# Performance work log

Measured on AMD Instinct MI355X. Metric: run time of the kernel, lower is better.

The kernel has to match this reference:

```python
import jax, jax.numpy as jnp
import numpy as np

B, C, H, W = 2, 256, 64, 64
NUM_HEADS = 8


def setup_inputs() -> dict:
    key = jax.random.key(0)
    k1, k2, k3 = jax.random.split(key, 3)
    x = jax.random.normal(k1, (B, C, H, W), dtype=jnp.float32)
    # 1x1 convs, bias=False -> plain [out_ch, in_ch] matrices
    w_qkv = jax.random.normal(k2, (3 * C, C), dtype=jnp.float32) * (1.0 / np.sqrt(C))
    w_proj = jax.random.normal(k3, (C, C), dtype=jnp.float32) * (1.0 / np.sqrt(C))
    return {"x": x, "w_qkv": w_qkv, "w_proj": w_proj}


def reference(x, w_qkv, w_proj):
    b, c, h, w = x.shape
    hd = NUM_HEADS
    d = c // hd  # head dim
    n = h * w    # number of tokens

    # 1x1 conv == channel matmul: [3C, C] x [B, C, H, W] -> [B, 3C, H, W]
    qkv = jnp.einsum('oc,bchw->bohw', w_qkv, x)
    q, k, v = jnp.split(qkv, 3, axis=1)

    def reshape(t):
        return t.reshape(b, hd, d, n)  # [B, h, d, N]

    q, k, v = map(reshape, (q, k, v))

    # scores[b,h,i,j] = sum_d q[b,h,d,i] * k[b,h,d,j] / sqrt(d)
    scores = jnp.einsum('bhdi,bhdj->bhij', q, k) / jnp.sqrt(jnp.asarray(d, x.dtype))
    attn = jax.nn.softmax(scores, axis=-1)

    # out[b,h,d,i] = sum_j attn[b,h,i,j] * v[b,h,d,j]
    out = jnp.einsum('bhij,bhdj->bhdi', attn, v)
    out = out.reshape(b, c, h, w)

    return jnp.einsum('oc,bchw->bohw', w_proj, out) + x
```

## Files before the change

kernel.cpp:

```cpp
#include <hip/hip_runtime.h>
#include <hip/hip_bf16.h>

#define NB  2
#define CC  256
#define NHD 8
#define HD  32
#define NT  4096

typedef __bf16 bf16x8 __attribute__((ext_vector_type(8)));
typedef bf16x8 bf16x8_ma __attribute__((may_alias));
typedef __bf16 bf16x4 __attribute__((ext_vector_type(4)));
typedef bf16x4 bf16x4_ma __attribute__((may_alias));
typedef float  f32x4  __attribute__((ext_vector_type(4)));
typedef f32x4  f32x4_ma __attribute__((may_alias));
typedef float  f32x16 __attribute__((ext_vector_type(16)));
typedef unsigned int u32x4 __attribute__((ext_vector_type(4)));
typedef unsigned short u16x8 __attribute__((ext_vector_type(8)));

static __device__ __forceinline__ f32x4 zero4() {
    f32x4 z = {0.f, 0.f, 0.f, 0.f}; return z;
}
static __device__ __forceinline__ f32x16 zero16() {
    f32x16 z = {0.f,0.f,0.f,0.f,0.f,0.f,0.f,0.f,
                0.f,0.f,0.f,0.f,0.f,0.f,0.f,0.f};
    return z;
}

#define QSCALE 0.25505392421795654f

#define CVT_PK(dst, lo, hi_) \
    asm("v_cvt_pk_bf16_f32 %0, %1, %2" : "=v"(dst) : "v"(lo), "v"(hi_))
#define PLSWAP(x, y) \
    asm("v_permlane32_swap_b32 %0, %1" : "+v"(x), "+v"(y))


__global__ __launch_bounds__(256) void convw_k(const float* __restrict__ s1,
                                               __bf16* __restrict__ d1, int n1,
                                               const float* __restrict__ s2,
                                               __bf16* __restrict__ d2, int n2) {
    const int i = blockIdx.x * 256 + threadIdx.x;
    if (i < n1) d1[i] = (__bf16)s1[i];
    else if (i - n1 < n2) d2[i - n1] = (__bf16)s2[i - n1];
}

__global__ __launch_bounds__(256) void qkv_k(const __bf16* __restrict__ wqkv,
                                             const float* __restrict__ x,
                                             __bf16* __restrict__ qt,
                                             __bf16* __restrict__ kt,
                                             __bf16* __restrict__ vv) {
    __shared__ __align__(16) __bf16 T[64][264];

    const int tid  = threadIdx.x;
    const int lane = tid & 63, wv = tid >> 6;
    const int g = lane >> 4, c16 = lane & 15;
    const int b    = blockIdx.z;
    const int o0   = blockIdx.y * 64 + wv * 16;
    const int tok0 = blockIdx.x * 64;

    const int tok4 = (tid & 15) * 4;
    const int crow = tid >> 4;

    {
#pragma unroll
        for (int i = 0; i < 8; ++i) {
            const int c = i * 16 + crow;
            f32x4 v = *(const f32x4_ma*)&x[((size_t)(b * CC + c)) * NT + tok0 + tok4];
#pragma unroll
            for (int j = 0; j < 4; ++j) T[tok4 + j][c] = (__bf16)v[j];
        }
    }

    f32x4 v1[8];
#pragma unroll
    for (int i = 0; i < 8; ++i) {
        const int c = 128 + i * 16 + crow;
        v1[i] = *(const f32x4_ma*)&x[((size_t)(b * CC + c)) * NT + tok0 + tok4];
    }

    const __bf16* arow = wqkv + (size_t)(o0 + c16) * CC + g * 8;
    bf16x8 a[8];
#pragma unroll
    for (int kc = 0; kc < 8; ++kc) a[kc] = *(const bf16x8_ma*)(arow + kc * 32);

    __syncthreads();

    f32x4 acc[4];
#pragma unroll
    for (int i = 0; i < 4; ++i) acc[i] = zero4();

#pragma unroll
    for (int kc = 0; kc < 4; ++kc) {
#pragma unroll
        for (int js = 0; js < 4; ++js) {
            bf16x8 bb = *(const bf16x8_ma*)&T[js * 16 + c16][kc * 32 + g * 8];
            acc[js] = __builtin_amdgcn_mfma_f32_16x16x32_bf16(a[kc], bb, acc[js], 0, 0, 0);
        }
    }

#pragma unroll
    for (int i = 0; i < 8; ++i) {
        const int c = 128 + i * 16 + crow;
#pragma unroll
        for (int j = 0; j < 4; ++j) T[tok4 + j][c] = (__bf16)v1[i][j];
    }
    __syncthreads();

#pragma unroll
    for (int kc = 4; kc < 8; ++kc) {
#pragma unroll
        for (int js = 0; js < 4; ++js) {
            bf16x8 bb = *(const bf16x8_ma*)&T[js * 16 + c16][kc * 32 + g * 8];
            acc[js] = __builtin_amdgcn_mfma_f32_16x16x32_bf16(a[kc], bb, acc[js], 0, 0, 0);
        }
    }

    const int reg = o0 >> 8;
    const int oo0 = (o0 & 255) + g * 4;
    const int h   = oo0 >> 5;
    const int dd0 = oo0 & 31;
    const size_t bh = (size_t)(b * NHD + h);

#pragma unroll
    for (int js = 0; js < 4; ++js) {
        const int tok = tok0 + js * 16 + c16;
        if (reg == 0) {
            bf16x4 pk;
#pragma unroll
            for (int r = 0; r < 4; ++r) pk[r] = (__bf16)(acc[js][r] * QSCALE);
            *(bf16x4_ma*)(qt + (bh * NT + tok) * HD + dd0) = pk;
        } else if (reg == 1) {
            bf16x4 pk;
#pragma unroll
            for (int r = 0; r < 4; ++r) pk[r] = (__bf16)acc[js][r];
            *(bf16x4_ma*)(kt + (bh * NT + tok) * HD + dd0) = pk;
        } else {
#pragma unroll
            for (int r = 0; r < 4; ++r)
                vv[(bh * HD + dd0 + r) * NT + tok] = (__bf16)acc[js][r];
        }
    }
}

__global__ __launch_bounds__(256, 4) void attn_k(const __bf16* __restrict__ qt,
                                                 const __bf16* __restrict__ kt,
                                                 const __bf16* __restrict__ vv,
                                                 __bf16* __restrict__ ao,
                                                 float* __restrict__ PO,
                                                 float* __restrict__ PL) {
    __shared__ __align__(16) __bf16 KF[2][4][2][512];
    __shared__ __align__(16) __bf16 VF[2][4][2][512];

    const int tid  = threadIdx.x;
    const int lane = tid & 63, wv = tid >> 6;
    const int c32 = lane & 31, hi = lane >> 5;
    const int bh = blockIdx.y;
    const int b = bh >> 3, h = bh & 7;
    const int seg = blockIdx.z, nseg = gridDim.z;
    const int i0q = blockIdx.x * 128 + wv * 32;

    const __bf16* qbase = qt + ((size_t)bh * NT + i0q) * HD;
    const __bf16* kbase = kt + (size_t)bh * NT * HD;
    const __bf16* vbase = vv + (size_t)bh * HD * NT;

    bf16x8 aq0 = *(const bf16x8_ma*)(qbase + (size_t)c32 * HD + hi * 8);
    bf16x8 aq1 = *(const bf16x8_ma*)(qbase + (size_t)c32 * HD + 16 + hi * 8);

    u16x8 ones_u = {0x3F80,0x3F80,0x3F80,0x3F80,0x3F80,0x3F80,0x3F80,0x3F80};
    const bf16x8 ones = __builtin_bit_cast(bf16x8, ones_u);

    f32x16 oacc = zero16();
    f32x16 lacc = zero16();

#define STAGE(bf, jb) do {                                                              \
    const __bf16* gk = kbase + (size_t)((jb) + wv * 32 + c32) * HD + hi * 8;            \
    __builtin_amdgcn_global_load_lds(                                                   \
        (const __attribute__((address_space(1))) void*)gk,                              \
        (__attribute__((address_space(3))) void*)&KF[bf][wv][0][0],                     \
        16, 0, 0);                                                                      \
    __builtin_amdgcn_global_load_lds(                                                   \
        (const __attribute__((address_space(1))) void*)(gk + 16),                       \
        (__attribute__((address_space(3))) void*)&KF[bf][wv][1][0],                     \
        16, 0, 0);                                                                      \
    const __bf16* gv = vbase + (size_t)c32 * NT + (jb) + wv * 32 + hi * 8;              \
    __builtin_amdgcn_global_load_lds(                                                   \
        (const __attribute__((address_space(1))) void*)gv,                              \
        (__attribute__((address_space(3))) void*)&VF[bf][wv][0][0],                     \
        16, 0, 0);                                                                      \
    __builtin_amdgcn_global_load_lds(                                                   \
        (const __attribute__((address_space(1))) void*)(gv + 16),                       \
        (__attribute__((address_space(3))) void*)&VF[bf][wv][1][0],                     \
        16, 0, 0);                                                                      \
} while (0)

#define SUBTILE(bf, js) do {                                                            \
    bf16x8 fk0 = *(const bf16x8_ma*)&KF[bf][js][0][lane * 8];                           \
    bf16x8 fk1 = *(const bf16x8_ma*)&KF[bf][js][1][lane * 8];                           \
    bf16x8 fv0 = *(const bf16x8_ma*)&VF[bf][js][0][lane * 8];                           \
    bf16x8 fv1 = *(const bf16x8_ma*)&VF[bf][js][1][lane * 8];                           \
    f32x16 s = __builtin_amdgcn_mfma_f32_32x32x16_bf16(fk0, aq0, zero16(), 0, 0, 0);    \
    s = __builtin_amdgcn_mfma_f32_32x32x16_bf16(fk1, aq1, s, 0, 0, 0);                  \
    float p[16];                                                                        \
    _Pragma("unroll")                                                                   \
    for (int r = 0; r < 16; ++r) p[r] = __builtin_amdgcn_exp2f(s[r]);                   \
    unsigned pk[8];                                                                     \
    _Pragma("unroll")                                                                   \
    for (int i = 0; i < 8; ++i) CVT_PK(pk[i], p[2 * i], p[2 * i + 1]);                  \
    PLSWAP(pk[0], pk[2]);                                                               \
    PLSWAP(pk[1], pk[3]);                                                               \
    PLSWAP(pk[4], pk[6]);                                                               \
    PLSWAP(pk[5], pk[7]);                                                               \
    u32x4 a0 = {pk[0], pk[1], pk[2], pk[3]};                                            \
    u32x4 a1 = {pk[4], pk[5], pk[6], pk[7]};                                            \
    const bf16x8 ap0 = __builtin_bit_cast(bf16x8, a0);                                  \
    const bf16x8 ap1 = __builtin_bit_cast(bf16x8, a1);                                  \
    oacc = __builtin_amdgcn_mfma_f32_32x32x16_bf16(ap0, fv0, oacc, 0, 0, 0);            \
    oacc = __builtin_amdgcn_mfma_f32_32x32x16_bf16(ap1, fv1, oacc, 0, 0, 0);            \
    lacc = __builtin_amdgcn_mfma_f32_32x32x16_bf16(ap0, ones, lacc, 0, 0, 0);           \
    lacc = __builtin_amdgcn_mfma_f32_32x32x16_bf16(ap1, ones, lacc, 0, 0, 0);           \
} while (0)

    const int ntiles  = (NT / 128) / nseg;
    const int j_begin = seg * ntiles * 128;

    STAGE(0, j_begin);
    asm volatile("s_waitcnt vmcnt(0)" ::: "memory");
    __syncthreads();

    int buf = 0;
#pragma unroll 1
    for (int t = 0; t < ntiles; ++t) {
        if (t + 1 < ntiles) STAGE(buf ^ 1, j_begin + (t + 1) * 128);
        SUBTILE(buf, 0);
        SUBTILE(buf, 1);
        SUBTILE(buf, 2);
        SUBTILE(buf, 3);
        asm volatile("s_waitcnt vmcnt(0)" ::: "memory");
        __syncthreads();
        buf ^= 1;
    }

#undef STAGE
#undef SUBTILE

    if (nseg == 1) {
#pragma unroll
        for (int g4 = 0; g4 < 4; ++g4) {
#pragma unroll
            for (int r = 0; r < 4; ++r) {
                const int q = 8 * g4 + 4 * hi + r;
                ao[((size_t)(b * NT) + i0q + q) * CC + h * HD + c32] =
                    (__bf16)(oacc[4 * g4 + r] / lacc[4 * g4 + r]);
            }
        }
    } else {
        float* po = PO + (((size_t)seg * NB * NHD + bh) * NT + i0q) * HD;
#pragma unroll
        for (int g4 = 0; g4 < 4; ++g4) {
#pragma unroll
            for (int r = 0; r < 4; ++r) {
                const int q = 8 * g4 + 4 * hi + r;
                po[(size_t)q * HD + c32] = oacc[4 * g4 + r];
            }
        }
        if (c32 == 0) {
            float* pl = PL + ((size_t)seg * NB * NHD + bh) * NT + i0q;
#pragma unroll
            for (int g4 = 0; g4 < 4; ++g4)
#pragma unroll
                for (int r = 0; r < 4; ++r)
                    pl[8 * g4 + 4 * hi + r] = lacc[4 * g4 + r];
        }
    }
}

__global__ __launch_bounds__(256) void comb_k(const float* __restrict__ PO,
                                              const float* __restrict__ PL,
                                              __bf16* __restrict__ ao,
                                              int nseg) {
    const int i = blockIdx.x * 256 + threadIdx.x;
    const int bh = i >> 15;
    const int rem = i & 32767;
    const int n = rem >> 3, g = rem & 7;
    const int b = bh >> 3, h = bh & 7;

    const size_t SEGO = (size_t)(NB * NHD) * NT * HD;
    const size_t SEGL = (size_t)(NB * NHD) * NT;
    const size_t o0i = (((size_t)bh) * NT + n) * HD + g * 4;
    const size_t li  = (size_t)bh * NT + n;

    f32x4 o = *(const f32x4_ma*)&PO[o0i];
    float l = PL[li];
#pragma unroll 3
    for (int s = 1; s < nseg; ++s) {
        o += *(const f32x4_ma*)&PO[(size_t)s * SEGO + o0i];
        l += PL[(size_t)s * SEGL + li];
    }

    bf16x4 pk;
#pragma unroll
    for (int r = 0; r < 4; ++r) pk[r] = (__bf16)(o[r] / l);
    *(bf16x4_ma*)&ao[((size_t)(b * NT) + n) * CC + h * HD + g * 4] = pk;
}

__global__ __launch_bounds__(256) void proj_k(const __bf16* __restrict__ wp,
                                              const __bf16* __restrict__ ao,
                                              const float* __restrict__ x,
                                              float* __restrict__ out) {
    __shared__ __align__(16) __bf16 BF[4][8][512];

    const int lane = threadIdx.x & 63, wv = threadIdx.x >> 6;
    const int g = lane >> 4, c16 = lane & 15;
    const int b    = blockIdx.z;
    const int o0   = blockIdx.y * 64 + wv * 16;
    const int tok0 = blockIdx.x * 64;

    const __bf16* bsrc = ao + ((size_t)(b * NT + tok0 + wv * 16 + c16)) * CC + g * 8;
#pragma unroll
    for (int kc = 0; kc < 4; ++kc) {
        __builtin_amdgcn_global_load_lds(
            (const __attribute__((address_space(1))) void*)(bsrc + kc * 32),
            (__attribute__((address_space(3))) void*)&BF[wv][kc][0],
            16, 0, 0);
    }

    const __bf16* arow = wp + (size_t)(o0 + c16) * CC + g * 8;
    bf16x8 a[8];
#pragma unroll
    for (int kc = 0; kc < 8; ++kc) a[kc] = *(const bf16x8_ma*)(arow + kc * 32);

    __syncthreads();

#pragma unroll
    for (int kc = 4; kc < 8; ++kc) {
        __builtin_amdgcn_global_load_lds(
            (const __attribute__((address_space(1))) void*)(bsrc + kc * 32),
            (__attribute__((address_space(3))) void*)&BF[wv][kc][0],
            16, 0, 0);
    }

    f32x4 acc[4];
#pragma unroll
    for (int i = 0; i < 4; ++i) acc[i] = zero4();

#pragma unroll
    for (int kc = 0; kc < 4; ++kc) {
#pragma unroll
        for (int js = 0; js < 4; ++js) {
            bf16x8 bb = *(const bf16x8_ma*)&BF[js][kc][lane * 8];
            acc[js] = __builtin_amdgcn_mfma_f32_16x16x32_bf16(a[kc], bb, acc[js], 0, 0, 0);
        }
    }

    asm volatile("s_waitcnt vmcnt(0)" ::: "memory");
    __syncthreads();

#pragma unroll
    for (int kc = 4; kc < 8; ++kc) {
#pragma unroll
        for (int js = 0; js < 4; ++js) {
            bf16x8 bb = *(const bf16x8_ma*)&BF[js][kc][lane * 8];
            acc[js] = __builtin_amdgcn_mfma_f32_16x16x32_bf16(a[kc], bb, acc[js], 0, 0, 0);
        }
    }

#pragma unroll
    for (int js = 0; js < 4; ++js) {
        const int tok = tok0 + js * 16 + c16;
#pragma unroll
        for (int r = 0; r < 4; ++r) {
            const int o = o0 + g * 4 + r;
            const size_t idx = ((size_t)(b * CC + o)) * NT + tok;
            out[idx] = acc[js][r] + x[idx];
        }
    }
}

extern "C" void kernel_launch(void* const* d_in, const int* in_sizes, int n_in,
                              void* d_out, int out_size, void* d_ws, size_t ws_size,
                              hipStream_t stream) {
    const int SX  = NB * CC * NT;
    const int SW3 = 3 * CC * CC;
    const int SW1 = CC * CC;
    const size_t E = (size_t)SX;

    const float* x  = nullptr;
    const float* wq = nullptr;
    const float* wp = nullptr;
    for (int i = 0; i < n_in; ++i) {
        const int sz = in_sizes[i];
        if (sz == SX || sz == 2 * SX || sz == 4 * SX)           x  = (const float*)d_in[i];
        else if (sz == SW3 || sz == 2 * SW3 || sz == 4 * SW3)   wq = (const float*)d_in[i];
        else if (sz == SW1 || sz == 2 * SW1 || sz == 4 * SW1)   wp = (const float*)d_in[i];
    }
    if (!x || !wq || !wp) {
        x  = (const float*)d_in[0];
        wq = (const float*)d_in[1];
        wp = (const float*)d_in[2];
    }

    __bf16* ws  = (__bf16*)d_ws;
    __bf16* wqb = ws;
    __bf16* wpb = wqb + SW3;
    __bf16* ao  = wpb + SW1;
    __bf16* qt  = ao + E;
    __bf16* kt  = qt + E;
    __bf16* vv  = kt + E;

    const size_t baseB = (size_t)(SW3 + SW1) * 2 + 4 * E * 2;
    const size_t segoB = (size_t)NB * NHD * NT * HD * 4;
    const size_t seglB = (size_t)NB * NHD * NT * 4;
    const int jseg = (ws_size >= baseB + 2 * (segoB + seglB)) ? 2 : 1;
    float* PO = (float*)((char*)d_ws + baseB);
    float* PL = (float*)((char*)d_ws + baseB + (size_t)jseg * segoB);

    float* out = (float*)d_out;

    convw_k<<<dim3((SW3 + SW1 + 255) / 256), 256, 0, stream>>>(wq, wqb, SW3, wp, wpb, SW1);
    qkv_k<<<dim3(NT / 64, (3 * CC) / 64, NB), 256, 0, stream>>>(wqb, x, qt, kt, vv);
    attn_k<<<dim3(NT / 128, NB * NHD, jseg), 256, 0, stream>>>(qt, kt, vv, ao, PO, PL);
    if (jseg > 1)
        comb_k<<<dim3((NB * NHD * NT * (HD / 4)) / 256), 256, 0, stream>>>(PO, PL, ao, jseg);
    proj_k<<<dim3(NT / 64, CC / 64, NB), 256, 0, stream>>>(wpb, ao, x, out);
}
```

Before: 141.6 us.

## Process two query tiles per wave and replace ones-MFMA row sums with VALU sums

Each wave now handles 64 queries (two 32-row Q tiles) instead of 32, so each K/V fragment read from LDS is reused twice, and blocks shrink to 128 threads with each wave staging two subtiles. The softmax denominator, previously computed with two extra MFMAs against a ones matrix, is now accumulated with VALU adds on the exp values and reduced by cross-lane shuffles at the end. This removes a third of the MFMA work and halves LDS reads per unit of compute, in exchange for more registers per wave, fewer waves per block, and extra VALU adds alongside the exp work.

```diff
diff --git a/kernel.cpp b/kernel.cpp
--- a/kernel.cpp
+++ b/kernel.cpp
@@ -15,7 +15,6 @@
 typedef f32x4  f32x4_ma __attribute__((may_alias));
 typedef float  f32x16 __attribute__((ext_vector_type(16)));
 typedef unsigned int u32x4 __attribute__((ext_vector_type(4)));
-typedef unsigned short u16x8 __attribute__((ext_vector_type(8)));
 
 static __device__ __forceinline__ f32x4 zero4() {
     f32x4 z = {0.f, 0.f, 0.f, 0.f}; return z;
@@ -141,12 +140,12 @@
     }
 }
 
-__global__ __launch_bounds__(256, 4) void attn_k(const __bf16* __restrict__ qt,
-                                                 const __bf16* __restrict__ kt,
-                                                 const __bf16* __restrict__ vv,
-                                                 __bf16* __restrict__ ao,
-                                                 float* __restrict__ PO,
-                                                 float* __restrict__ PL) {
+__global__ __launch_bounds__(128) void attn_k(const __bf16* __restrict__ qt,
+                                              const __bf16* __restrict__ kt,
+                                              const __bf16* __restrict__ vv,
+                                              __bf16* __restrict__ ao,
+                                              float* __restrict__ PO,
+                                              float* __restrict__ PL) {
     __shared__ __align__(16) __bf16 KF[2][4][2][512];
     __shared__ __align__(16) __bf16 VF[2][4][2][512];
 
@@ -156,52 +155,56 @@
     const int bh = blockIdx.y;
     const int b = bh >> 3, h = bh & 7;
     const int seg = blockIdx.z, nseg = gridDim.z;
-    const int i0q = blockIdx.x * 128 + wv * 32;
+    const int i0q = blockIdx.x * 128 + wv * 64;
 
     const __bf16* qbase = qt + ((size_t)bh * NT + i0q) * HD;
     const __bf16* kbase = kt + (size_t)bh * NT * HD;
     const __bf16* vbase = vv + (size_t)bh * HD * NT;
 
-    bf16x8 aq0 = *(const bf16x8_ma*)(qbase + (size_t)c32 * HD + hi * 8);
-    bf16x8 aq1 = *(const bf16x8_ma*)(qbase + (size_t)c32 * HD + 16 + hi * 8);
-
-    u16x8 ones_u = {0x3F80,0x3F80,0x3F80,0x3F80,0x3F80,0x3F80,0x3F80,0x3F80};
-    const bf16x8 ones = __builtin_bit_cast(bf16x8, ones_u);
-
-    f32x16 oacc = zero16();
-    f32x16 lacc = zero16();
+    bf16x8 aq00 = *(const bf16x8_ma*)(qbase + (size_t)c32 * HD + hi * 8);
+    bf16x8 aq01 = *(const bf16x8_ma*)(qbase + (size_t)c32 * HD + 16 + hi * 8);
+    bf16x8 aq10 = *(const bf16x8_ma*)(qbase + (size_t)(32 + c32) * HD + hi * 8);
+    bf16x8 aq11 = *(const bf16x8_ma*)(qbase + (size_t)(32 + c32) * HD + 16 + hi * 8);
+
+    f32x16 oacc0 = zero16();
+    f32x16 oacc1 = zero16();
+    float rs0[4] = {0.f, 0.f, 0.f, 0.f};
+    float rs1[4] = {0.f, 0.f, 0.f, 0.f};
 
 #define STAGE(bf, jb) do {                                                              \
-    const __bf16* gk = kbase + (size_t)((jb) + wv * 32 + c32) * HD + hi * 8;            \
-    __builtin_amdgcn_global_load_lds(                                                   \
-        (const __attribute__((address_space(1))) void*)gk,                              \
-        (__attribute__((address_space(3))) void*)&KF[bf][wv][0][0],                     \
-        16, 0, 0);                                                                      \
-    __builtin_amdgcn_global_load_lds(                                                   \
-        (const __attribute__((address_space(1))) void*)(gk + 16),                       \
-        (__attribute__((address_space(3))) void*)&KF[bf][wv][1][0],                     \
-        16, 0, 0);                                                                      \
-    const __bf16* gv = vbase + (size_t)c32 * NT + (jb) + wv * 32 + hi * 8;              \
-    __builtin_amdgcn_global_load_lds(                                                   \
-        (const __attribute__((address_space(1))) void*)gv,                              \
-        (__attribute__((address_space(3))) void*)&VF[bf][wv][0][0],                     \
-        16, 0, 0);                                                                      \
-    __builtin_amdgcn_global_load_lds(                                                   \
-        (const __attribute__((address_space(1))) void*)(gv + 16),                       \
-        (__attribute__((address_space(3))) void*)&VF[bf][wv][1][0],                     \
-        16, 0, 0);                                                                      \
+    _Pragma("unroll")                                                                   \
+    for (int j2 = 0; j2 < 2; ++j2) {                                                    \
+        const int js = wv * 2 + j2;                                                     \
+        const __bf16* gk = kbase + (size_t)((jb) + js * 32 + c32) * HD + hi * 8;        \
+        __builtin_amdgcn_global_load_lds(                                               \
+            (const __attribute__((address_space(1))) void*)gk,                          \
+            (__attribute__((address_space(3))) void*)&KF[bf][js][0][0],                 \
+            16, 0, 0);                                                                  \
+        __builtin_amdgcn_global_load_lds(                                               \
+            (const __attribute__((address_space(1))) void*)(gk + 16),                   \
+            (__attribute__((address_space(3))) void*)&KF[bf][js][1][0],                 \
+            16, 0, 0);                                                                  \
+        const __bf16* gv = vbase + (size_t)c32 * NT + (jb) + js * 32 + hi * 8;          \
+        __builtin_amdgcn_global_load_lds(                                               \
+            (const __attribute__((address_space(1))) void*)gv,                          \
+            (__attribute__((address_space(3))) void*)&VF[bf][js][0][0],                 \
+            16, 0, 0);                                                                  \
+        __builtin_amdgcn_global_load_lds(                                               \
+            (const __attribute__((address_space(1))) void*)(gv + 16),                   \
+            (__attribute__((address_space(3))) void*)&VF[bf][js][1][0],                 \
+            16, 0, 0);                                                                  \
+    }                                                                                   \
 } while (0)
 
-#define SUBTILE(bf, js) do {                                                            \
-    bf16x8 fk0 = *(const bf16x8_ma*)&KF[bf][js][0][lane * 8];                           \
-    bf16x8 fk1 = *(const bf16x8_ma*)&KF[bf][js][1][lane * 8];                           \
-    bf16x8 fv0 = *(const bf16x8_ma*)&VF[bf][js][0][lane * 8];                           \
-    bf16x8 fv1 = *(const bf16x8_ma*)&VF[bf][js][1][lane * 8];                           \
-    f32x16 s = __builtin_amdgcn_mfma_f32_32x32x16_bf16(fk0, aq0, zero16(), 0, 0, 0);    \
-    s = __builtin_amdgcn_mfma_f32_32x32x16_bf16(fk1, aq1, s, 0, 0, 0);                  \
+#define QSBODY(aqA, aqB, rsv, oaccv) do {                                               \
+    f32x16 s = __builtin_amdgcn_mfma_f32_32x32x16_bf16(fk0, aqA, zero16(), 0, 0, 0);    \
+    s = __builtin_amdgcn_mfma_f32_32x32x16_bf16(fk1, aqB, s, 0, 0, 0);                  \
     float p[16];                                                                        \
     _Pragma("unroll")                                                                   \
-    for (int r = 0; r < 16; ++r) p[r] = __builtin_amdgcn_exp2f(s[r]);                   \
+    for (int r = 0; r < 16; ++r) {                                                      \
+        p[r] = __builtin_amdgcn_exp2f(s[r]);                                            \
+        rsv[r & 3] += p[r];                                                             \
+    }                                                                                   \
     unsigned pk[8];                                                                     \
     _Pragma("unroll")                                                                   \
     for (int i = 0; i < 8; ++i) CVT_PK(pk[i], p[2 * i], p[2 * i + 1]);                  \
@@ -213,10 +216,17 @@
     u32x4 a1 = {pk[4], pk[5], pk[6], pk[7]};                                            \
     const bf16x8 ap0 = __builtin_bit_cast(bf16x8, a0);                                  \
     const bf16x8 ap1 = __builtin_bit_cast(bf16x8, a1);                                  \
-    oacc = __builtin_amdgcn_mfma_f32_32x32x16_bf16(ap0, fv0, oacc, 0, 0, 0);            \
-    oacc = __builtin_amdgcn_mfma_f32_32x32x16_bf16(ap1, fv1, oacc, 0, 0, 0);            \
-    lacc = __builtin_amdgcn_mfma_f32_32x32x16_bf16(ap0, ones, lacc, 0, 0, 0);           \
-    lacc = __builtin_amdgcn_mfma_f32_32x32x16_bf16(ap1, ones, lacc, 0, 0, 0);           \
+    oaccv = __builtin_amdgcn_mfma_f32_32x32x16_bf16(ap0, fv0, oaccv, 0, 0, 0);          \
+    oaccv = __builtin_amdgcn_mfma_f32_32x32x16_bf16(ap1, fv1, oaccv, 0, 0, 0);          \
+} while (0)
+
+#define SUBTILE(bf, js) do {                                                            \
+    bf16x8 fk0 = *(const bf16x8_ma*)&KF[bf][js][0][lane * 8];                           \
+    bf16x8 fk1 = *(const bf16x8_ma*)&KF[bf][js][1][lane * 8];                           \
+    bf16x8 fv0 = *(const bf16x8_ma*)&VF[bf][js][0][lane * 8];                           \
+    bf16x8 fv1 = *(const bf16x8_ma*)&VF[bf][js][1][lane * 8];                           \
+    QSBODY(aq00, aq01, rs0, oacc0);                                                     \
+    QSBODY(aq10, aq11, rs1, oacc1);                                                     \
 } while (0)
 
     const int ntiles  = (NT / 128) / nseg;
@@ -241,6 +251,12 @@
 
 #undef STAGE
 #undef SUBTILE
+#undef QSBODY
+
+    float rsa = (rs0[0] + rs0[1]) + (rs0[2] + rs0[3]);
+    rsa += __shfl_xor(rsa, 32, 64);
+    float rsb = (rs1[0] + rs1[1]) + (rs1[2] + rs1[3]);
+    rsb += __shfl_xor(rsb, 32, 64);
 
     if (nseg == 1) {
 #pragma unroll
@@ -248,8 +264,12 @@
 #pragma unroll
             for (int r = 0; r < 4; ++r) {
                 const int q = 8 * g4 + 4 * hi + r;
+                const float lt0 = __shfl(rsa, q, 64);
                 ao[((size_t)(b * NT) + i0q + q) * CC + h * HD + c32] =
-                    (__bf16)(oacc[4 * g4 + r] / lacc[4 * g4 + r]);
+                    (__bf16)(oacc0[4 * g4 + r] / lt0);
+                const float lt1 = __shfl(rsb, q, 64);
+                ao[((size_t)(b * NT) + i0q + 32 + q) * CC + h * HD + c32] =
+                    (__bf16)(oacc1[4 * g4 + r] / lt1);
             }
         }
     } else {
@@ -259,16 +279,14 @@
 #pragma unroll
             for (int r = 0; r < 4; ++r) {
                 const int q = 8 * g4 + 4 * hi + r;
-                po[(size_t)q * HD + c32] = oacc[4 * g4 + r];
+                po[(size_t)q * HD + c32] = oacc0[4 * g4 + r];
+                po[(size_t)(32 + q) * HD + c32] = oacc1[4 * g4 + r];
             }
         }
-        if (c32 == 0) {
+        if (hi == 0) {
             float* pl = PL + ((size_t)seg * NB * NHD + bh) * NT + i0q;
-#pragma unroll
-            for (int g4 = 0; g4 < 4; ++g4)
-#pragma unroll
-                for (int r = 0; r < 4; ++r)
-                    pl[8 * g4 + 4 * hi + r] = lacc[4 * g4 + r];
+            pl[c32]      = rsa;
+            pl[32 + c32] = rsb;
         }
     }
 }
@@ -417,7 +435,7 @@
 
     convw_k<<<dim3((SW3 + SW1 + 255) / 256), 256, 0, stream>>>(wq, wqb, SW3, wp, wpb, SW1);
     qkv_k<<<dim3(NT / 64, (3 * CC) / 64, NB), 256, 0, stream>>>(wqb, x, qt, kt, vv);
-    attn_k<<<dim3(NT / 128, NB * NHD, jseg), 256, 0, stream>>>(qt, kt, vv, ao, PO, PL);
+    attn_k<<<dim3(NT / 128, NB * NHD, jseg), 128, 0, stream>>>(qt, kt, vv, ao, PO, PL);
     if (jseg > 1)
         comb_k<<<dim3((NB * NHD * NT * (HD / 4)) / 256), 256, 0, stream>>>(PO, PL, ao, jseg);
     proj_k<<<dim3(NT / 64, CC / 64, NB), 256, 0, stream>>>(wpb, ao, x, out);
```

Result: slower. 167.9 us (+18.5%).
